# Optimization experiments

Measured on AMD Instinct MI355X. Metric: run time of the kernel, lower is better.

Reference implementation:

```python
import jax, jax.numpy as jnp
import numpy as np


def _conv1x1(x, w, b):
    # x: [B,C,H,W], w: [Cout,Cin], b: [Cout]  (1x1 conv == per-pixel linear)
    return jnp.einsum('bchw,oc->bohw', x, w) + b[None, :, None, None]


def setup_inputs() -> dict:
    key = jax.random.key(0)
    ks = jax.random.split(key, 8)
    B, C, H, W = 8, 128, 128, 128
    s = 1.0 / np.sqrt(C)
    return {
        'q_feat': jax.random.normal(ks[0], (B, C, H, W), jnp.float32),
        'kv_feat': jax.random.normal(ks[1], (B, C, H, W), jnp.float32),
        'q_w': jax.random.normal(ks[2], (C, C), jnp.float32) * s,
        'q_b': jax.random.normal(ks[3], (C,), jnp.float32) * 0.01,
        'k_w': jax.random.normal(ks[4], (C, C), jnp.float32) * s,
        'k_b': jax.random.normal(ks[5], (C,), jnp.float32) * 0.01,
        'v_w': jax.random.normal(ks[6], (C, C), jnp.float32) * s,
        'v_b': jax.random.normal(ks[7], (C,), jnp.float32) * 0.01,
    }


def reference(q_feat, kv_feat, q_w, q_b, k_w, k_b, v_w, v_b):
    B, C, H, W = q_feat.shape
    q = _conv1x1(q_feat, q_w, q_b).reshape(B, C, H * W)   # [B,C,N]
    k = _conv1x1(kv_feat, k_w, k_b).reshape(B, C, H * W)  # [B,C,N]
    v = _conv1x1(kv_feat, v_w, v_b).reshape(B, C, H * W)  # [B,C,N]
    k_sm = jax.nn.softmax(k, axis=-1)                     # softmax over spatial dim N
    context = jnp.einsum('bcn,bdn->bcd', v, k_sm)         # [B,C,C]
    out = jnp.einsum('bcd,bdn->bcn', context, q)          # [B,C,N]
    return out.reshape(B, C, H, W)
```

## Files before the change

kernel.cpp:

```cpp
#include <hip/hip_runtime.h>
#include <hip/hip_bf16.h>
#include <cstdint>

#define B_ 8
#define C_ 128
#define N_ 16384
#define CHN 512
#define SN 128
#define NST 4
#define NC (N_ / CHN)

typedef __attribute__((ext_vector_type(8))) short short8;
typedef __attribute__((ext_vector_type(4))) float f32x4;
typedef __attribute__((ext_vector_type(4))) unsigned short us4;
typedef unsigned short u16;

__device__ __forceinline__ short f2bf(float f) {
  union { float f; unsigned u; } c; c.f = f;
  unsigned r = (c.u + 0x7FFFu + ((c.u >> 16) & 1u)) >> 16;
  return (short)r;
}

__device__ __forceinline__ unsigned cvtpk(float lo, float hi) {
  unsigned r;
  asm("v_cvt_pk_bf16_f32 %0, %1, %2" : "=v"(r) : "v"(lo), "v"(hi));
  return r;
}

union SB { short8 s8; unsigned u[4]; };

__global__ __launch_bounds__(256) void k0_wcvt(const float* __restrict__ kw,
                                               const float* __restrict__ vw,
                                               u16* __restrict__ wbf) {
  const int g = blockIdx.x * 256 + threadIdx.x;
  const int mat = g >> 12, o4 = g & 4095;
  const float* src = mat ? vw : kw;
  float4 f = reinterpret_cast<const float4*>(src)[o4];
  us4 s;
  s[0] = (u16)f2bf(f.x); s[1] = (u16)f2bf(f.y);
  s[2] = (u16)f2bf(f.z); s[3] = (u16)f2bf(f.w);
  reinterpret_cast<us4*>(wbf + (size_t)mat * C_ * C_)[o4] = s;
}

#define STAGE_LOADS(BASE_, ST_) do {                                         \
  _Pragma("unroll") for (int i_ = 0; i_ < 8; ++i_)                           \
    xf[i_] = *reinterpret_cast<const f32x4*>(                                \
        (BASE_) + (size_t)((lane >> 5) * 8 + i_) * N_ + (ST_) * SN +         \
        (lane & 31) * 4);                                                    \
} while (0)

#define STAGE_XWRITE(BUF_) do {                                              \
  const int db_ = w * 16 + (lane >> 5) * 8;                                  \
  _Pragma("unroll") for (int k_ = 0; k_ < 4; ++k_) {                         \
    const int n_ = (lane & 31) * 4 + k_;                                     \
    uint4 q_;                                                                \
    q_.x = cvtpk(xf[0][k_], xf[1][k_]);                                      \
    q_.y = cvtpk(xf[2][k_], xf[3][k_]);                                      \
    q_.z = cvtpk(xf[4][k_], xf[5][k_]);                                      \
    q_.w = cvtpk(xf[6][k_], xf[7][k_]);                                      \
    *reinterpret_cast<uint4*>(                                               \
        (BUF_) + n_ * SN + (db_ ^ ((n_ & 7) << 3))) = q_;                    \
  }                                                                          \
} while (0)

__global__ __launch_bounds__(512, 2) void ka_projctx(
    const float* __restrict__ kv, const u16* __restrict__ wbf,
    const float* __restrict__ kb, const float* __restrict__ vb,
    float* __restrict__ part, float* __restrict__ zpart) {
  __shared__ u16 xt[2][C_ * SN];
  __shared__ u16 eks[C_ * SN];
  __shared__ u16 vs [C_ * SN];

  const int fid = blockIdx.x + blockIdx.y * NC;
  const int fid2 = (fid & 7) * 32 + (fid >> 3);
  const int b = fid2 >> 5, kc = fid2 & 31;
  const int tid = threadIdx.x;
  const int w = tid >> 6, lane = tid & 63;
  const int lg = lane >> 4, li = lane & 15;
  const int mat = w >> 2, dblk = w & 3;
  const int cg = w >> 1, dh = w & 1;

  const float* xb = kv + (size_t)b * C_ * N_ + (size_t)kc * CHN;
  const float* xw = xb + (size_t)(w * 16) * N_;
  const u16* Wm = wbf + (size_t)mat * C_ * C_;
  const float* biasp = mat ? vb : kb;
  u16* S = mat ? vs : eks;

  short8 wreg[2][4];
#pragma unroll
  for (int dt = 0; dt < 2; ++dt)
#pragma unroll
    for (int ks = 0; ks < 4; ++ks)
      wreg[dt][ks] = *reinterpret_cast<const short8*>(
          Wm + (dblk * 32 + dt * 16 + li) * C_ + ks * 32 + lg * 8);
  float bias2[2];
#pragma unroll
  for (int dt = 0; dt < 2; ++dt) bias2[dt] = biasp[dblk * 32 + dt * 16 + li];

  f32x4 acc[2][4] = {};
  float zac[2] = {0.f, 0.f};
  f32x4 xf[8];

  STAGE_LOADS(xw, 0);
  STAGE_XWRITE(&xt[0][0]);
  STAGE_LOADS(xw, 1);
  asm volatile("s_waitcnt lgkmcnt(0)" ::: "memory");
  __builtin_amdgcn_s_barrier();
  __builtin_amdgcn_sched_barrier(0);

#pragma unroll
  for (int st = 0; st < NST; ++st) {
    const u16* xc = &xt[st & 1][0];

    if (st < NST - 1) {
      STAGE_XWRITE(&xt[(st + 1) & 1][0]);
      if (st < NST - 2) STAGE_LOADS(xw, st + 2);
    }

#pragma unroll
    for (int h2 = 0; h2 < 4; ++h2) {
      f32x4 pacc[2][2] = {};
#pragma unroll
      for (int ntl = 0; ntl < 2; ++ntl) {
        const int n = (h2 * 2 + ntl) * 16 + li;
#pragma unroll
        for (int ks = 0; ks < 4; ++ks) {
          short8 a = *reinterpret_cast<const short8*>(
              xc + n * SN + ((ks * 32 + lg * 8) ^ ((n & 7) << 3)));
#pragma unroll
          for (int dt = 0; dt < 2; ++dt)
            pacc[ntl][dt] = __builtin_amdgcn_mfma_f32_16x16x32_bf16(
                a, wreg[dt][ks], pacc[ntl][dt], 0, 0, 0);
        }
      }
#pragma unroll
      for (int dt = 0; dt < 2; ++dt) {
        const int d = dblk * 32 + dt * 16 + li;
        const float bias = bias2[dt];
#pragma unroll
        for (int ntl = 0; ntl < 2; ++ntl) {
          float v0 = pacc[ntl][dt][0] + bias;
          float v1 = pacc[ntl][dt][1] + bias;
          float v2 = pacc[ntl][dt][2] + bias;
          float v3 = pacc[ntl][dt][3] + bias;
          if (mat == 0) {
            v0 = __expf(v0); v1 = __expf(v1); v2 = __expf(v2); v3 = __expf(v3);
            zac[dt] += (v0 + v1) + (v2 + v3);
          }
          const int nq = (h2 * 2 + ntl) * 16 + lg * 4;
          uint2 pk; pk.x = cvtpk(v0, v1); pk.y = cvtpk(v2, v3);
          *reinterpret_cast<uint2*>(S + d * SN + (nq ^ ((d & 7) << 3))) = pk;
        }
      }
    }
    asm volatile("s_waitcnt lgkmcnt(0)" ::: "memory");
    __builtin_amdgcn_s_barrier();
    __builtin_amdgcn_sched_barrier(0);

#pragma unroll
    for (int kk = 0; kk < 4; ++kk) {
      const int n0 = kk * 32 + lg * 8;
      short8 a[2], bb[4];
#pragma unroll
      for (int am = 0; am < 2; ++am) {
        const int c = cg * 32 + am * 16 + li;
        a[am] = *reinterpret_cast<const short8*>(vs + c * SN + (n0 ^ ((c & 7) << 3)));
      }
#pragma unroll
      for (int dt = 0; dt < 4; ++dt) {
        const int d = dh * 64 + dt * 16 + li;
        bb[dt] = *reinterpret_cast<const short8*>(eks + d * SN + (n0 ^ ((d & 7) << 3)));
      }
#pragma unroll
      for (int am = 0; am < 2; ++am)
#pragma unroll
        for (int dt = 0; dt < 4; ++dt)
          acc[am][dt] = __builtin_amdgcn_mfma_f32_16x16x32_bf16(a[am], bb[dt], acc[am][dt], 0, 0, 0);
    }
    asm volatile("s_waitcnt lgkmcnt(0)" ::: "memory");
    __builtin_amdgcn_s_barrier();
    __builtin_amdgcn_sched_barrier(0);
  }

  float* P = part + ((size_t)kc * B_ + b) * C_ * C_;
#pragma unroll
  for (int am = 0; am < 2; ++am)
#pragma unroll
    for (int dt = 0; dt < 4; ++dt)
#pragma unroll
      for (int r = 0; r < 4; ++r) {
        const int c = cg * 32 + am * 16 + lg * 4 + r;
        const int d = dh * 64 + dt * 16 + li;
        P[c * C_ + d] = acc[am][dt][r];
      }
  if (mat == 0) {
#pragma unroll
    for (int dt = 0; dt < 2; ++dt) {
      float z = zac[dt];
      z += __shfl_xor(z, 16);
      z += __shfl_xor(z, 32);
      if (lg == 0)
        zpart[((size_t)kc * B_ + b) * C_ + dblk * 32 + dt * 16 + li] = z;
    }
  }
}

__global__ __launch_bounds__(256) void kb2_fin(
    const float* __restrict__ part, const float* __restrict__ zpart,
    const float* __restrict__ qw, const float* __restrict__ qb,
    u16* __restrict__ M, float* __restrict__ T) {
  const int b = blockIdx.y;
  const int cs0 = blockIdx.x * 16;
  const int tid = threadIdx.x;
  __shared__ float cs[16][128];
  __shared__ float Zs[128];
  if (tid < 128) {
    float s = 0.f;
    for (int kc = 0; kc < NC; ++kc)
      s += zpart[((size_t)kc * B_ + b) * C_ + tid];
    Zs[tid] = s;
  }
  __syncthreads();
#pragma unroll
  for (int i = 0; i < 8; ++i) {
    const int e = tid + i * 256;
    const int cl = e >> 7, d = e & 127;
    float s = 0.f;
    for (int kc = 0; kc < NC; ++kc)
      s += part[(((size_t)kc * B_ + b) * C_ + (cs0 + cl)) * C_ + d];
    cs[cl][d] = s / Zs[d];
  }
  __syncthreads();
  const int cl = tid >> 4, e0 = (tid & 15) * 8;
  float m[8] = {};
  for (int d = 0; d < 128; ++d) {
    const float cv = cs[cl][d];
    const float* qr = qw + d * C_ + e0;
#pragma unroll
    for (int j = 0; j < 8; ++j) m[j] += cv * qr[j];
  }
  u16* mp = M + ((size_t)b * C_ + cs0 + cl) * C_ + e0;
#pragma unroll
  for (int j = 0; j < 8; ++j) mp[j] = (u16)f2bf(m[j]);
  if (tid < 16) {
    float tv = 0.f;
    for (int d = 0; d < 128; ++d) tv += cs[tid][d] * qb[d];
    T[b * C_ + cs0 + tid] = tv;
  }
}

__global__ __launch_bounds__(512) void k4_out(const u16* __restrict__ M,
                                              const float* __restrict__ T,
                                              const float* __restrict__ q,
                                              float* __restrict__ out) {
  __shared__ u16 qt[2][SN * C_];

  const int fid = blockIdx.x + blockIdx.y * NC;
  const int fid2 = (fid & 7) * 32 + (fid >> 3);
  const int b = fid2 >> 5, kc = fid2 & 31;
  const int nb = kc * CHN;
  const int tid = threadIdx.x;
  const int w = tid >> 6, lane = tid & 63;
  const int lg = lane >> 4, li = lane & 15;

  const float* qw_ = q + (size_t)b * C_ * N_ + nb + (size_t)(w * 16) * N_;

  short8 mreg[4];
  const u16* Mb = M + (size_t)b * C_ * C_;
#pragma unroll
  for (int ks = 0; ks < 4; ++ks)
    mreg[ks] = *reinterpret_cast<const short8*>(
        Mb + (w * 16 + li) * C_ + ks * 32 + lg * 8);
  float tcv[4];
#pragma unroll
  for (int r = 0; r < 4; ++r) tcv[r] = T[b * C_ + w * 16 + lg * 4 + r];

  f32x4 xf[8];
  f32x4 acc[NST][8] = {};

  STAGE_LOADS(qw_, 0);
  STAGE_XWRITE(&qt[0][0]);
  STAGE_LOADS(qw_, 1);
  asm volatile("s_waitcnt lgkmcnt(0)" ::: "memory");
  __builtin_amdgcn_s_barrier();
  __builtin_amdgcn_sched_barrier(0);

#pragma unroll
  for (int st = 0; st < NST; ++st) {
    const u16* xc = &qt[st & 1][0];

    if (st < NST - 1) {
      STAGE_XWRITE(&qt[(st + 1) & 1][0]);
      if (st < NST - 2) STAGE_LOADS(qw_, st + 2);
    }

#pragma unroll
    for (int nt = 0; nt < 8; ++nt) {
      const int n = nt * 16 + li;
#pragma unroll
      for (int ks = 0; ks < 4; ++ks) {
        short8 bb = *reinterpret_cast<const short8*>(
            xc + n * SN + ((ks * 32 + lg * 8) ^ ((n & 7) << 3)));
        acc[st][nt] = __builtin_amdgcn_mfma_f32_16x16x32_bf16(
            mreg[ks], bb, acc[st][nt], 0, 0, 0);
      }
    }

    asm volatile("s_waitcnt lgkmcnt(0)" ::: "memory");
    __builtin_amdgcn_s_barrier();
    __builtin_amdgcn_sched_barrier(0);
  }

#pragma unroll
  for (int r = 0; r < 4; ++r) {
    const int c = w * 16 + lg * 4 + r;
    float* op = out + ((size_t)b * C_ + c) * N_ + nb;
    const float t = tcv[r];
#pragma unroll
    for (int st = 0; st < NST; ++st)
#pragma unroll
      for (int nt = 0; nt < 8; ++nt)
        op[st * SN + nt * 16 + li] = acc[st][nt][r] + t;
  }
}

extern "C" void kernel_launch(void* const* d_in, const int* in_sizes, int n_in,
                              void* d_out, int out_size, void* d_ws, size_t ws_size,
                              hipStream_t stream) {
  const float* q_feat  = (const float*)d_in[0];
  const float* kv_feat = (const float*)d_in[1];
  const float* q_w = (const float*)d_in[2];
  const float* q_b = (const float*)d_in[3];
  const float* k_w = (const float*)d_in[4];
  const float* k_b = (const float*)d_in[5];
  const float* v_w = (const float*)d_in[6];
  const float* v_b = (const float*)d_in[7];
  float* out = (float*)d_out;

  char* ws = (char*)d_ws;
  const size_t szPart = (size_t)NC * B_ * C_ * C_ * sizeof(float);
  const size_t szZp   = (size_t)NC * B_ * C_ * sizeof(float);
  const size_t szWbf  = (size_t)2 * C_ * C_ * sizeof(u16);
  const size_t szM    = (size_t)B_ * C_ * C_ * sizeof(u16);

  float* part  = (float*)ws;
  float* zpart = (float*)(ws + szPart);
  u16*   wbf   = (u16*)(ws + szPart + szZp);
  u16*   M     = (u16*)(ws + szPart + szZp + szWbf);
  float* T     = (float*)(ws + szPart + szZp + szWbf + szM);

  k0_wcvt<<<dim3(32), 256, 0, stream>>>(k_w, v_w, wbf);
  ka_projctx<<<dim3(NC, B_), 512, 0, stream>>>(kv_feat, wbf, k_b, v_b, part, zpart);
  kb2_fin<<<dim3(8, B_), 256, 0, stream>>>(part, zpart, q_w, q_b, M, T);
  k4_out<<<dim3(NC, B_), 512, 0, stream>>>(M, T, q_feat, out);
}
```

Baseline: 74.39 us.

## Split output kernel into smaller 128-column blocks with 4 waves each

The final out = M·q kernel now launches 1024 blocks of 256 threads, each covering one 128-pixel tile, instead of 256 blocks of 512 threads that each looped over four tiles with a double-buffered LDS pipeline. Each wave now computes 32 output channels (two M row tiles) and reuses every LDS B-fragment across two MFMAs. This is meant to raise occupancy and spread work across more CUs, with the grid-level overlap replacing the in-kernel software pipeline. The cost is more blocks that each repeat the M and T register loads, and no explicit overlap of global loads with compute inside a block.

```diff
diff --git a/kernel.cpp b/kernel.cpp
--- a/kernel.cpp
+++ b/kernel.cpp
@@ -249,79 +249,91 @@
   }
 }
 
-__global__ __launch_bounds__(512) void k4_out(const u16* __restrict__ M,
+#define K4_LOADS(H_) do {                                                    \
+  _Pragma("unroll") for (int i_ = 0; i_ < 8; ++i_)                           \
+    xf[i_] = *reinterpret_cast<const f32x4*>(                                \
+        qsrc + (size_t)((H_) * 16 + (lane >> 5) * 8 + i_) * N_ +             \
+        (lane & 31) * 4);                                                    \
+} while (0)
+
+#define K4_XWRITE(H_) do {                                                   \
+  const int db_ = w * 32 + (H_) * 16 + (lane >> 5) * 8;                      \
+  _Pragma("unroll") for (int k_ = 0; k_ < 4; ++k_) {                         \
+    const int n_ = (lane & 31) * 4 + k_;                                     \
+    uint4 q_;                                                                \
+    q_.x = cvtpk(xf[0][k_], xf[1][k_]);                                      \
+    q_.y = cvtpk(xf[2][k_], xf[3][k_]);                                      \
+    q_.z = cvtpk(xf[4][k_], xf[5][k_]);                                      \
+    q_.w = cvtpk(xf[6][k_], xf[7][k_]);                                      \
+    *reinterpret_cast<uint4*>(                                               \
+        qt + n_ * SN + (db_ ^ ((n_ & 7) << 3))) = q_;                        \
+  }                                                                          \
+} while (0)
+
+__global__ __launch_bounds__(256) void k4_out(const u16* __restrict__ M,
                                               const float* __restrict__ T,
                                               const float* __restrict__ q,
                                               float* __restrict__ out) {
-  __shared__ u16 qt[2][SN * C_];
-
-  const int fid = blockIdx.x + blockIdx.y * NC;
-  const int fid2 = (fid & 7) * 32 + (fid >> 3);
-  const int b = fid2 >> 5, kc = fid2 & 31;
-  const int nb = kc * CHN;
+  __shared__ u16 qt[SN * C_];
+
+  const int fid = blockIdx.x + blockIdx.y * 128;
+  const int fid2 = (fid & 7) * 128 + (fid >> 3);
+  const int b = fid2 >> 7, nc = fid2 & 127;
+  const int nb = nc * SN;
   const int tid = threadIdx.x;
   const int w = tid >> 6, lane = tid & 63;
   const int lg = lane >> 4, li = lane & 15;
 
-  const float* qw_ = q + (size_t)b * C_ * N_ + nb + (size_t)(w * 16) * N_;
-
-  short8 mreg[4];
+  const float* qsrc = q + (size_t)b * C_ * N_ + nb + (size_t)(w * 32) * N_;
+
+  short8 mreg[2][4];
   const u16* Mb = M + (size_t)b * C_ * C_;
 #pragma unroll
-  for (int ks = 0; ks < 4; ++ks)
-    mreg[ks] = *reinterpret_cast<const short8*>(
-        Mb + (w * 16 + li) * C_ + ks * 32 + lg * 8);
-  float tcv[4];
-#pragma unroll
-  for (int r = 0; r < 4; ++r) tcv[r] = T[b * C_ + w * 16 + lg * 4 + r];
+  for (int ct = 0; ct < 2; ++ct)
+#pragma unroll
+    for (int ks = 0; ks < 4; ++ks)
+      mreg[ct][ks] = *reinterpret_cast<const short8*>(
+          Mb + (w * 32 + ct * 16 + li) * C_ + ks * 32 + lg * 8);
+  float tcv[2][4];
+#pragma unroll
+  for (int ct = 0; ct < 2; ++ct)
+#pragma unroll
+    for (int r = 0; r < 4; ++r)
+      tcv[ct][r] = T[b * C_ + w * 32 + ct * 16 + lg * 4 + r];
 
   f32x4 xf[8];
-  f32x4 acc[NST][8] = {};
-
-  STAGE_LOADS(qw_, 0);
-  STAGE_XWRITE(&qt[0][0]);
-  STAGE_LOADS(qw_, 1);
-  asm volatile("s_waitcnt lgkmcnt(0)" ::: "memory");
-  __builtin_amdgcn_s_barrier();
-  __builtin_amdgcn_sched_barrier(0);
-
-#pragma unroll
-  for (int st = 0; st < NST; ++st) {
-    const u16* xc = &qt[st & 1][0];
-
-    if (st < NST - 1) {
-      STAGE_XWRITE(&qt[(st + 1) & 1][0]);
-      if (st < NST - 2) STAGE_LOADS(qw_, st + 2);
-    }
-
-#pragma unroll
-    for (int nt = 0; nt < 8; ++nt) {
-      const int n = nt * 16 + li;
-#pragma unroll
-      for (int ks = 0; ks < 4; ++ks) {
-        short8 bb = *reinterpret_cast<const short8*>(
-            xc + n * SN + ((ks * 32 + lg * 8) ^ ((n & 7) << 3)));
-        acc[st][nt] = __builtin_amdgcn_mfma_f32_16x16x32_bf16(
-            mreg[ks], bb, acc[st][nt], 0, 0, 0);
-      }
-    }
-
-    asm volatile("s_waitcnt lgkmcnt(0)" ::: "memory");
-    __builtin_amdgcn_s_barrier();
-    __builtin_amdgcn_sched_barrier(0);
-  }
-
-#pragma unroll
-  for (int r = 0; r < 4; ++r) {
-    const int c = w * 16 + lg * 4 + r;
-    float* op = out + ((size_t)b * C_ + c) * N_ + nb;
-    const float t = tcv[r];
-#pragma unroll
-    for (int st = 0; st < NST; ++st)
+  K4_LOADS(0);
+  K4_XWRITE(0);
+  K4_LOADS(1);
+  K4_XWRITE(1);
+  __syncthreads();
+
+  f32x4 acc[2][8] = {};
+#pragma unroll
+  for (int nt = 0; nt < 8; ++nt) {
+    const int n = nt * 16 + li;
+#pragma unroll
+    for (int ks = 0; ks < 4; ++ks) {
+      short8 bb = *reinterpret_cast<const short8*>(
+          qt + n * SN + ((ks * 32 + lg * 8) ^ ((n & 7) << 3)));
+#pragma unroll
+      for (int ct = 0; ct < 2; ++ct)
+        acc[ct][nt] = __builtin_amdgcn_mfma_f32_16x16x32_bf16(
+            mreg[ct][ks], bb, acc[ct][nt], 0, 0, 0);
+    }
+  }
+
+#pragma unroll
+  for (int ct = 0; ct < 2; ++ct)
+#pragma unroll
+    for (int r = 0; r < 4; ++r) {
+      const int c = w * 32 + ct * 16 + lg * 4 + r;
+      float* op = out + ((size_t)b * C_ + c) * N_ + nb;
+      const float t = tcv[ct][r];
 #pragma unroll
       for (int nt = 0; nt < 8; ++nt)
-        op[st * SN + nt * 16 + li] = acc[st][nt][r] + t;
-  }
+        op[nt * 16 + li] = acc[ct][nt][r] + t;
+    }
 }
 
 extern "C" void kernel_launch(void* const* d_in, const int* in_sizes, int n_in,
@@ -352,5 +364,5 @@
   k0_wcvt<<<dim3(32), 256, 0, stream>>>(k_w, v_w, wbf);
   ka_projctx<<<dim3(NC, B_), 512, 0, stream>>>(kv_feat, wbf, k_b, v_b, part, zpart);
   kb2_fin<<<dim3(8, B_), 256, 0, stream>>>(part, zpart, q_w, q_b, M, T);
-  k4_out<<<dim3(NC, B_), 512, 0, stream>>>(M, T, q_feat, out);
-}
+  k4_out<<<dim3(128, B_), 256, 0, stream>>>(M, T, q_feat, out);
+}
```

New measurement: 72.89 us. -2.0%, faster.
